# Kernel optimization log

Measured on AMD Instinct MI355X. Metric: run time of the kernel, lower is better.

Reference implementation:

```python
import jax, jax.numpy as jnp
import numpy as np

N = 100000
E = 1600000
D_IN = 128
D_H = 128
BN_EPS = 1e-5


def setup_inputs() -> dict:
    key = jax.random.key(0)
    ks = jax.random.split(key, 8)
    x = jax.random.normal(ks[0], (N, D_IN), dtype=jnp.float32)
    edge_index = jax.random.randint(ks[1], (2, E), 0, N, dtype=jnp.int64)
    # MLP params (Linear stores weight as [out, in])
    lim1 = 1.0 / np.sqrt(D_IN)
    W1 = jax.random.uniform(ks[2], (D_H, D_IN), minval=-lim1, maxval=lim1, dtype=jnp.float32)
    b1 = jax.random.uniform(ks[3], (D_H,), minval=-lim1, maxval=lim1, dtype=jnp.float32)
    gamma = jnp.ones((D_H,), dtype=jnp.float32)
    beta = jnp.zeros((D_H,), dtype=jnp.float32)
    lim2 = 1.0 / np.sqrt(D_H)
    W2 = jax.random.uniform(ks[4], (D_H, D_H), minval=-lim2, maxval=lim2, dtype=jnp.float32)
    b2 = jax.random.uniform(ks[5], (D_H,), minval=-lim2, maxval=lim2, dtype=jnp.float32)
    eps = jnp.float32(0.0)  # trainable eps parameter, init 0
    return {"x": x, "edge_index": edge_index, "eps": eps, "W1": W1, "b1": b1,
            "gamma": gamma, "beta": beta, "W2": W2, "b2": b2}


def reference(x, edge_index, eps, W1, b1, gamma, beta, W2, b2):
    src = edge_index[0]
    dst = edge_index[1]
    # Augmented edges = original + reversed + self-loops.
    # aggr[dst] += x[src]; aggr[src] += x[dst]; aggr[i] += x[i]
    aggr = jnp.zeros_like(x).at[dst].add(x[src]).at[src].add(x[dst]) + x
    h = (1.0 + eps) * x + aggr              # [N, D_IN]
    h = h @ W1.T + b1                        # [N, D_H]
    # BatchNorm1d in training mode: batch stats, biased variance
    mean = jnp.mean(h, axis=0)
    var = jnp.mean(jnp.square(h - mean), axis=0)
    h = gamma * (h - mean) * jax.lax.rsqrt(var + BN_EPS) + beta
    h = jax.nn.relu(h)
    return h @ W2.T + b2                     # [N, D_H]
```

## Files before the change

kernel.cpp:

```cpp
#include <hip/hip_runtime.h>
#include <hip/hip_fp16.h>

#define N_NODES 100000
#define EDGES   1600000
#define D       128
#define BN_EPS  1e-5f
#define TM      64
#define NT      ((N_NODES + TM - 1) / TM)
#define GGRID   782
#define NB      782
#define SLOT    4800
#define L1E     8
#define L1TILE  (256 * L1E)
#define GBLKS   1536
#define GWAVES  (GBLKS * 4)
#define NREP    32

typedef __attribute__((ext_vector_type(8))) short short8;
typedef __attribute__((ext_vector_type(4))) float f32x4;

__device__ __forceinline__ unsigned short bf_hi(float f) {
    unsigned u = __float_as_uint(f);
    unsigned t = u + 0x7FFF + ((u >> 16) & 1);
    return (unsigned short)(t >> 16);
}
__device__ __forceinline__ float bf_val(unsigned short h) {
    return __uint_as_float(((unsigned)h) << 16);
}
__device__ __forceinline__ void split8(const float* __restrict__ p, short8* hi, short8* lo) {
    short8 h, l;
#pragma unroll
    for (int i = 0; i < 8; ++i) {
        float f = p[i];
        unsigned short hh = bf_hi(f);
        ((unsigned short*)&h)[i] = (short)hh;
        ((unsigned short*)&l)[i] = (short)bf_hi(f - bf_val(hh));
    }
    *hi = h; *lo = l;
}

__launch_bounds__(256)
__global__ void fused_pg(const float* __restrict__ x,
                         const float* __restrict__ W1,
                         __half* __restrict__ yh,
                         const int* __restrict__ ei, int* __restrict__ gcur,
                         int* __restrict__ pairs) {
    __shared__ unsigned short sH[TM][136];
    __shared__ unsigned short sL[TM][136];
    const int tid = threadIdx.x;

    if (blockIdx.x >= GGRID) {
        int* cnt   = (int*)&sH[0][0];
        int* cbase = cnt + NB;
        for (int i = tid; i < NB; i += 256) cnt[i] = 0;
        __syncthreads();

        int bbA[L1E], rrA[L1E], pkA[L1E];
        int bbB[L1E], rrB[L1E], pkB[L1E];
        const int t0 = (blockIdx.x - GGRID) * L1TILE + tid;
#pragma unroll
        for (int j = 0; j < L1E; ++j) {
            int t = t0 + j * 256;
            bbA[j] = -1;
            bbB[j] = -1;
            if (t < EDGES) {
                int s = ei[t];
                int d = ei[EDGES + t];
                bbA[j] = d >> 7;
                pkA[j] = ((d & 127) << 17) | s;
                rrA[j] = atomicAdd(&cnt[bbA[j]], 1);
                bbB[j] = s >> 7;
                pkB[j] = ((s & 127) << 17) | d;
                rrB[j] = atomicAdd(&cnt[bbB[j]], 1);
            }
        }
        __syncthreads();
        for (int i = tid; i < NB; i += 256) {
            int c = cnt[i];
            cbase[i] = c ? (i * SLOT + atomicAdd(&gcur[i], c)) : 0;
        }
        __syncthreads();
#pragma unroll
        for (int j = 0; j < L1E; ++j) {
            if (bbA[j] >= 0) {
                pairs[cbase[bbA[j]] + rrA[j]] = pkA[j];
                pairs[cbase[bbB[j]] + rrB[j]] = pkB[j];
            }
        }
        return;
    }

    const int wv  = tid >> 6;
    const int ln  = tid & 63;
    const int lc  = ln & 15;
    const int qd  = ln >> 4;
    const int sr  = tid >> 5;
    const int sc4 = tid & 31;

    short8 Bh[4][2], Bl[4][2];
#pragma unroll
    for (int kk = 0; kk < 4; ++kk)
#pragma unroll
        for (int tl = 0; tl < 2; ++tl) {
            int woff = (wv * 32 + tl * 16 + lc) * D + kk * 32 + qd * 8;
            split8(W1 + woff, &Bh[kk][tl], &Bl[kk][tl]);
        }

    float4 pf[8];
    int tile = blockIdx.x;
#pragma unroll
    for (int i = 0; i < 8; ++i) {
        int gr = tile * TM + sr + i * 8;
        pf[i] = make_float4(0.f, 0.f, 0.f, 0.f);
        if (gr < N_NODES)
            pf[i] = *(const float4*)(x + (long long)gr * D + sc4 * 4);
    }

    while (tile < NT) {
#pragma unroll
        for (int i = 0; i < 8; ++i) {
            float4 v = pf[i];
            unsigned short h0 = bf_hi(v.x), h1b = bf_hi(v.y), h2 = bf_hi(v.z), h3 = bf_hi(v.w);
            unsigned short l0 = bf_hi(v.x - bf_val(h0)), l1 = bf_hi(v.y - bf_val(h1b));
            unsigned short l2 = bf_hi(v.z - bf_val(h2)), l3 = bf_hi(v.w - bf_val(h3));
            int r = sr + i * 8;
            *(uint2*)&sH[r][sc4 * 4] = make_uint2((unsigned)h0 | ((unsigned)h1b << 16),
                                                  (unsigned)h2 | ((unsigned)h3 << 16));
            *(uint2*)&sL[r][sc4 * 4] = make_uint2((unsigned)l0 | ((unsigned)l1 << 16),
                                                  (unsigned)l2 | ((unsigned)l3 << 16));
        }
        __syncthreads();
        int nxt = tile + GGRID;
        if (nxt < NT) {
#pragma unroll
            for (int i = 0; i < 8; ++i) {
                int gr = nxt * TM + sr + i * 8;
                pf[i] = make_float4(0.f, 0.f, 0.f, 0.f);
                if (gr < N_NODES)
                    pf[i] = *(const float4*)(x + (long long)gr * D + sc4 * 4);
            }
        }

        f32x4 acc[4][2];
#pragma unroll
        for (int m = 0; m < 4; ++m)
#pragma unroll
            for (int tl = 0; tl < 2; ++tl) acc[m][tl] = (f32x4){0.f, 0.f, 0.f, 0.f};

#pragma unroll
        for (int kk = 0; kk < 4; ++kk) {
#pragma unroll
            for (int m = 0; m < 4; ++m) {
                short8 ah = *(const short8*)&sH[m * 16 + lc][kk * 32 + qd * 8];
                short8 al = *(const short8*)&sL[m * 16 + lc][kk * 32 + qd * 8];
#pragma unroll
                for (int tl = 0; tl < 2; ++tl) {
                    acc[m][tl] = __builtin_amdgcn_mfma_f32_16x16x32_bf16(ah, Bh[kk][tl], acc[m][tl], 0, 0, 0);
                    acc[m][tl] = __builtin_amdgcn_mfma_f32_16x16x32_bf16(al, Bh[kk][tl], acc[m][tl], 0, 0, 0);
                    acc[m][tl] = __builtin_amdgcn_mfma_f32_16x16x32_bf16(ah, Bl[kk][tl], acc[m][tl], 0, 0, 0);
                }
            }
        }

        const int row0 = tile * TM;
#pragma unroll
        for (int m = 0; m < 4; ++m)
#pragma unroll
            for (int tl = 0; tl < 2; ++tl) {
                int col = wv * 32 + tl * 16 + lc;
#pragma unroll
                for (int r = 0; r < 4; ++r) {
                    int grow = row0 + m * 16 + qd * 4 + r;
                    if (grow < N_NODES)
                        yh[(long long)grow * D + col] = __float2half(acc[m][tl][r]);
                }
            }
        __syncthreads();
        tile = nxt;
    }
}

__launch_bounds__(256)
__global__ void bucket_fill(int* __restrict__ pairs, const int* __restrict__ gcur,
                            int* __restrict__ ofs, int* __restrict__ oen) {
    __shared__ int sP[SLOT];
    __shared__ int lc[128];
    __shared__ int cur[128];
    const int b    = blockIdx.x;
    const int tid  = threadIdx.x;
    const int base = b * SLOT;
    const int m    = min(gcur[b], SLOT);
    for (int i = tid; i < m; i += 256) sP[i] = pairs[base + i];
    if (tid < 128) lc[tid] = 0;
    __syncthreads();
    for (int i = tid; i < m; i += 256) atomicAdd(&lc[sP[i] >> 17], 1);
    __syncthreads();
    int v = (tid < 128) ? lc[tid] : 0;
    for (int d = 1; d < 128; d <<= 1) {
        int u = (tid >= d && tid < 128) ? lc[tid - d] : 0;
        __syncthreads();
        if (tid < 128) lc[tid] += u;
        __syncthreads();
    }
    if (tid < 128) {
        int abs0 = base + lc[tid] - v;
        cur[tid] = abs0;
        const int n = (b << 7) + tid;
        if (n < N_NODES) { ofs[n] = abs0; oen[n] = abs0 + v; }
    }
    __syncthreads();
    for (int i = tid; i < m; i += 256) {
        int p = sP[i];
        int r = atomicAdd(&cur[p >> 17], 1);
        pairs[r] = p & 0x1FFFF;
    }
}

__launch_bounds__(256)
__global__ void gather_aggr(const __half* __restrict__ yh,
                            const int* __restrict__ adj, const int* __restrict__ ofs,
                            const int* __restrict__ oen, const float* __restrict__ eps_p,
                            const float* __restrict__ b1,
                            float* __restrict__ h1, float* __restrict__ stats) {
    const int wv   = threadIdx.x >> 6;
    const int lane = threadIdx.x & 63;
    const int wave = blockIdx.x * 4 + wv;
    const __half2* xp = (const __half2*)yh;
    const float sc = 2.0f + eps_p[0];
    const float2 b1c = ((const float2*)b1)[lane];
    float sx = 0.f, sy = 0.f, qx = 0.f, qy = 0.f;

    for (int node = wave; node < N_NODES; node += GWAVES) {
        int b = ofs[node];
        int e = oen[node];
        float ax = 0.f, ay = 0.f;
        int i = b;
        for (; i + 8 <= e; i += 8) {
            int n0 = adj[i],     n1 = adj[i + 1], n2 = adj[i + 2], n3 = adj[i + 3];
            int n4 = adj[i + 4], n5 = adj[i + 5], n6 = adj[i + 6], n7 = adj[i + 7];
            __half2 v0 = xp[(unsigned)n0 * 64u + lane];
            __half2 v1 = xp[(unsigned)n1 * 64u + lane];
            __half2 v2 = xp[(unsigned)n2 * 64u + lane];
            __half2 v3 = xp[(unsigned)n3 * 64u + lane];
            __half2 v4 = xp[(unsigned)n4 * 64u + lane];
            __half2 v5 = xp[(unsigned)n5 * 64u + lane];
            __half2 v6 = xp[(unsigned)n6 * 64u + lane];
            __half2 v7 = xp[(unsigned)n7 * 64u + lane];
            float2 f0 = __half22float2(v0);
            float2 f1 = __half22float2(v1);
            float2 f2 = __half22float2(v2);
            float2 f3 = __half22float2(v3);
            float2 f4 = __half22float2(v4);
            float2 f5 = __half22float2(v5);
            float2 f6 = __half22float2(v6);
            float2 f7 = __half22float2(v7);
            ax += ((f0.x + f1.x) + (f2.x + f3.x)) + ((f4.x + f5.x) + (f6.x + f7.x));
            ay += ((f0.y + f1.y) + (f2.y + f3.y)) + ((f4.y + f5.y) + (f6.y + f7.y));
        }
        for (; i + 4 <= e; i += 4) {
            int n0 = adj[i], n1 = adj[i + 1], n2 = adj[i + 2], n3 = adj[i + 3];
            __half2 v0 = xp[(unsigned)n0 * 64u + lane];
            __half2 v1 = xp[(unsigned)n1 * 64u + lane];
            __half2 v2 = xp[(unsigned)n2 * 64u + lane];
            __half2 v3 = xp[(unsigned)n3 * 64u + lane];
            float2 f0 = __half22float2(v0);
            float2 f1 = __half22float2(v1);
            float2 f2 = __half22float2(v2);
            float2 f3 = __half22float2(v3);
            ax += (f0.x + f1.x) + (f2.x + f3.x);
            ay += (f0.y + f1.y) + (f2.y + f3.y);
        }
        for (; i < e; ++i) {
            __half2 v = xp[(unsigned)adj[i] * 64u + lane];
            float2 f = __half22float2(v);
            ax += f.x;
            ay += f.y;
        }
        float2 ys = __half22float2(xp[(unsigned)node * 64u + lane]);
        float ox = fmaf(sc, ys.x, ax) + b1c.x;
        float oy = fmaf(sc, ys.y, ay) + b1c.y;
        ((float2*)h1)[(long long)node * 64 + lane] = make_float2(ox, oy);
        sx += ox; sy += oy;
        qx += ox * ox; qy += oy * oy;
    }

    __shared__ float4 red[4][64];
    red[wv][lane] = make_float4(sx, sy, qx, qy);
    __syncthreads();
    if (wv == 0) {
        float4 a = red[0][lane], b4 = red[1][lane], c = red[2][lane], d4 = red[3][lane];
        float fx = (a.x + b4.x) + (c.x + d4.x);
        float fy = (a.y + b4.y) + (c.y + d4.y);
        float gx = (a.z + b4.z) + (c.z + d4.z);
        float gy = (a.w + b4.w) + (c.w + d4.w);
        float* st = stats + (blockIdx.x & (NREP - 1)) * 256;
        atomicAdd(&st[2 * lane],       fx);
        atomicAdd(&st[2 * lane + 1],   fy);
        atomicAdd(&st[128 + 2 * lane],     gx);
        atomicAdd(&st[128 + 2 * lane + 1], gy);
    }
}

__launch_bounds__(256)
__global__ void gemm2_mfma(float* __restrict__ h1out,
                           const float* __restrict__ W2,
                           const float* __restrict__ b2, const float* __restrict__ stats,
                           const float* __restrict__ gamma, const float* __restrict__ beta) {
    __shared__ unsigned short sH[TM][136];
    __shared__ unsigned short sL[TM][136];
    __shared__ float sScale[128];
    __shared__ float sShift[128];
    const int tid = threadIdx.x;
    const int wv  = tid >> 6;
    const int ln  = tid & 63;
    const int lc  = ln & 15;
    const int qd  = ln >> 4;
    const int sr  = tid >> 5;
    const int sc4 = tid & 31;

    if (tid < 128) {
        float s = 0.f, q = 0.f;
#pragma unroll
        for (int r = 0; r < NREP; ++r) {
            s += stats[r * 256 + tid];
            q += stats[r * 256 + 128 + tid];
        }
        float mean = s * (1.0f / N_NODES);
        float var  = fmaxf(q * (1.0f / N_NODES) - mean * mean, 0.0f);
        float sc   = gamma[tid] * rsqrtf(var + BN_EPS);
        sScale[tid] = sc;
        sShift[tid] = beta[tid] - mean * sc;
    }

    short8 Bh[4][2], Bl[4][2];
#pragma unroll
    for (int kk = 0; kk < 4; ++kk)
#pragma unroll
        for (int tl = 0; tl < 2; ++tl) {
            int woff = (wv * 32 + tl * 16 + lc) * D + kk * 32 + qd * 8;
            split8(W2 + woff, &Bh[kk][tl], &Bl[kk][tl]);
        }
    float bb[2];
    bb[0] = b2[wv * 32 + lc];
    bb[1] = b2[wv * 32 + 16 + lc];

    __syncthreads();

    float4 pf[8];
    int tile = blockIdx.x;
#pragma unroll
    for (int i = 0; i < 8; ++i) {
        int gr = tile * TM + sr + i * 8;
        pf[i] = make_float4(0.f, 0.f, 0.f, 0.f);
        if (gr < N_NODES)
            pf[i] = *(const float4*)(h1out + (long long)gr * D + sc4 * 4);
    }

    while (tile < NT) {
        float4 scv = *(const float4*)&sScale[sc4 * 4];
        float4 shv = *(const float4*)&sShift[sc4 * 4];
#pragma unroll
        for (int i = 0; i < 8; ++i) {
            int gr = tile * TM + sr + i * 8;
            float4 v = pf[i];
            if (gr < N_NODES) {
                v.x = fmaxf(0.f, fmaf(v.x, scv.x, shv.x));
                v.y = fmaxf(0.f, fmaf(v.y, scv.y, shv.y));
                v.z = fmaxf(0.f, fmaf(v.z, scv.z, shv.z));
                v.w = fmaxf(0.f, fmaf(v.w, scv.w, shv.w));
            } else {
                v = make_float4(0.f, 0.f, 0.f, 0.f);
            }
            unsigned short h0 = bf_hi(v.x), h1b = bf_hi(v.y), h2 = bf_hi(v.z), h3 = bf_hi(v.w);
            unsigned short l0 = bf_hi(v.x - bf_val(h0)), l1 = bf_hi(v.y - bf_val(h1b));
            unsigned short l2 = bf_hi(v.z - bf_val(h2)), l3 = bf_hi(v.w - bf_val(h3));
            int r = sr + i * 8;
            *(uint2*)&sH[r][sc4 * 4] = make_uint2((unsigned)h0 | ((unsigned)h1b << 16),
                                                  (unsigned)h2 | ((unsigned)h3 << 16));
            *(uint2*)&sL[r][sc4 * 4] = make_uint2((unsigned)l0 | ((unsigned)l1 << 16),
                                                  (unsigned)l2 | ((unsigned)l3 << 16));
        }
        __syncthreads();
        int nxt = tile + GGRID;
        if (nxt < NT) {
#pragma unroll
            for (int i = 0; i < 8; ++i) {
                int gr = nxt * TM + sr + i * 8;
                pf[i] = make_float4(0.f, 0.f, 0.f, 0.f);
                if (gr < N_NODES)
                    pf[i] = *(const float4*)(h1out + (long long)gr * D + sc4 * 4);
            }
        }

        f32x4 acc[4][2];
#pragma unroll
        for (int m = 0; m < 4; ++m)
#pragma unroll
            for (int tl = 0; tl < 2; ++tl) acc[m][tl] = (f32x4){0.f, 0.f, 0.f, 0.f};

#pragma unroll
        for (int kk = 0; kk < 4; ++kk) {
#pragma unroll
            for (int m = 0; m < 4; ++m) {
                short8 ah = *(const short8*)&sH[m * 16 + lc][kk * 32 + qd * 8];
                short8 al = *(const short8*)&sL[m * 16 + lc][kk * 32 + qd * 8];
#pragma unroll
                for (int tl = 0; tl < 2; ++tl) {
                    acc[m][tl] = __builtin_amdgcn_mfma_f32_16x16x32_bf16(ah, Bh[kk][tl], acc[m][tl], 0, 0, 0);
                    acc[m][tl] = __builtin_amdgcn_mfma_f32_16x16x32_bf16(al, Bh[kk][tl], acc[m][tl], 0, 0, 0);
                    acc[m][tl] = __builtin_amdgcn_mfma_f32_16x16x32_bf16(ah, Bl[kk][tl], acc[m][tl], 0, 0, 0);
                }
            }
        }

        const int row0 = tile * TM;
#pragma unroll
        for (int m = 0; m < 4; ++m)
#pragma unroll
            for (int tl = 0; tl < 2; ++tl) {
                int col = wv * 32 + tl * 16 + lc;
#pragma unroll
                for (int r = 0; r < 4; ++r) {
                    int grow = row0 + m * 16 + qd * 4 + r;
                    if (grow < N_NODES)
                        h1out[(long long)grow * D + col] = acc[m][tl][r] + bb[tl];
                }
            }
        __syncthreads();
        tile = nxt;
    }
}

extern "C" void kernel_launch(void* const* d_in, const int* in_sizes, int n_in,
                              void* d_out, int out_size, void* d_ws, size_t ws_size,
                              hipStream_t stream) {
    const float* x     = (const float*)d_in[0];
    const int*   ei    = (const int*)d_in[1];
    const float* eps_p = (const float*)d_in[2];
    const float* W1    = (const float*)d_in[3];
    const float* b1    = (const float*)d_in[4];
    const float* gamma = (const float*)d_in[5];
    const float* beta  = (const float*)d_in[6];
    const float* W2    = (const float*)d_in[7];
    const float* b2    = (const float*)d_in[8];

    __half* yh   = (__half*)d_ws;
    float*  stats = (float*)(yh + (long long)N_NODES * D);
    int*    gcur  = (int*)(stats + NREP * 256);
    int*    ofs   = gcur + 1024;
    int*    oen   = ofs + N_NODES;
    int*    pairs = (int*)(oen + N_NODES);
    int*    adj   = pairs;

    float* out = (float*)d_out;

    hipMemsetAsync(stats, 0, (NREP * 256 + 1024) * sizeof(int), stream);

    {
        fused_pg<<<GGRID + 782, 256, 0, stream>>>(x, W1, yh, ei, gcur, pairs);
    }
    {
        bucket_fill<<<NB, 256, 0, stream>>>(pairs, gcur, ofs, oen);
    }
    {
        gather_aggr<<<GBLKS, 256, 0, stream>>>(yh, adj, ofs, oen, eps_p, b1, out, stats);
    }
    {
        gemm2_mfma<<<GGRID, 256, 0, stream>>>(out, W2, b2, stats, gamma, beta);
    }
}
```

Baseline: 334.3 us.

## Fuse bucket sort and neighbor gather into one kernel using shared-memory adjacency

Merges the bucket_fill and gather_aggr kernels. Each 512-thread block now counting-sorts its bucket's pairs into LDS and immediately gathers neighbor features for its 128 nodes from there. This removes one launch, the global write and re-read of the adjacency and offset arrays, and the ofs/oen buffers. In exchange, gather parallelism is fixed at one block per 128 nodes (8 waves with 16 nodes each) rather than 1536 grid-strided blocks, which may lower memory-level parallelism and worsen load balance.

```diff
diff --git a/kernel.cpp b/kernel.cpp
--- a/kernel.cpp
+++ b/kernel.cpp
@@ -12,8 +12,6 @@
 #define SLOT    4800
 #define L1E     8
 #define L1TILE  (256 * L1E)
-#define GBLKS   1536
-#define GWAVES  (GBLKS * 4)
 #define NREP    32
 
 typedef __attribute__((ext_vector_type(8))) short short8;
@@ -180,20 +178,32 @@
     }
 }
 
-__launch_bounds__(256)
-__global__ void bucket_fill(int* __restrict__ pairs, const int* __restrict__ gcur,
-                            int* __restrict__ ofs, int* __restrict__ oen) {
-    __shared__ int sP[SLOT];
+__launch_bounds__(512)
+__global__ void bucket_gather(const __half* __restrict__ yh,
+                              const int* __restrict__ pairs, const int* __restrict__ gcur,
+                              const float* __restrict__ eps_p, const float* __restrict__ b1,
+                              float* __restrict__ h1, float* __restrict__ stats) {
+    __shared__ int sA[SLOT];
     __shared__ int lc[128];
     __shared__ int cur[128];
+    __shared__ int nofs[129];
+    __shared__ float4 red[8][64];
     const int b    = blockIdx.x;
     const int tid  = threadIdx.x;
     const int base = b * SLOT;
     const int m    = min(gcur[b], SLOT);
-    for (int i = tid; i < m; i += 256) sP[i] = pairs[base + i];
+
+    int my[10];
+#pragma unroll
+    for (int k = 0; k < 10; ++k) {
+        int i = tid + k * 512;
+        my[k] = (i < m) ? pairs[base + i] : -1;
+    }
     if (tid < 128) lc[tid] = 0;
     __syncthreads();
-    for (int i = tid; i < m; i += 256) atomicAdd(&lc[sP[i] >> 17], 1);
+#pragma unroll
+    for (int k = 0; k < 10; ++k)
+        if (my[k] >= 0) atomicAdd(&lc[my[k] >> 17], 1);
     __syncthreads();
     int v = (tid < 128) ? lc[tid] : 0;
     for (int d = 1; d < 128; d <<= 1) {
@@ -203,41 +213,37 @@
         __syncthreads();
     }
     if (tid < 128) {
-        int abs0 = base + lc[tid] - v;
-        cur[tid] = abs0;
-        const int n = (b << 7) + tid;
-        if (n < N_NODES) { ofs[n] = abs0; oen[n] = abs0 + v; }
-    }
-    __syncthreads();
-    for (int i = tid; i < m; i += 256) {
-        int p = sP[i];
-        int r = atomicAdd(&cur[p >> 17], 1);
-        pairs[r] = p & 0x1FFFF;
-    }
-}
-
-__launch_bounds__(256)
-__global__ void gather_aggr(const __half* __restrict__ yh,
-                            const int* __restrict__ adj, const int* __restrict__ ofs,
-                            const int* __restrict__ oen, const float* __restrict__ eps_p,
-                            const float* __restrict__ b1,
-                            float* __restrict__ h1, float* __restrict__ stats) {
-    const int wv   = threadIdx.x >> 6;
-    const int lane = threadIdx.x & 63;
-    const int wave = blockIdx.x * 4 + wv;
+        int e0 = lc[tid] - v;
+        cur[tid]  = e0;
+        nofs[tid] = e0;
+        if (tid == 127) nofs[128] = lc[127];
+    }
+    __syncthreads();
+#pragma unroll
+    for (int k = 0; k < 10; ++k)
+        if (my[k] >= 0) {
+            int r = atomicAdd(&cur[my[k] >> 17], 1);
+            sA[r] = my[k] & 0x1FFFF;
+        }
+    __syncthreads();
+
+    const int wv   = tid >> 6;
+    const int lane = tid & 63;
     const __half2* xp = (const __half2*)yh;
     const float sc = 2.0f + eps_p[0];
     const float2 b1c = ((const float2*)b1)[lane];
     float sx = 0.f, sy = 0.f, qx = 0.f, qy = 0.f;
 
-    for (int node = wave; node < N_NODES; node += GWAVES) {
-        int b = ofs[node];
-        int e = oen[node];
+    for (int ln = wv * 16; ln < wv * 16 + 16; ++ln) {
+        int node = (b << 7) + ln;
+        if (node >= N_NODES) break;
+        int nb = nofs[ln];
+        int ne = nofs[ln + 1];
         float ax = 0.f, ay = 0.f;
-        int i = b;
-        for (; i + 8 <= e; i += 8) {
-            int n0 = adj[i],     n1 = adj[i + 1], n2 = adj[i + 2], n3 = adj[i + 3];
-            int n4 = adj[i + 4], n5 = adj[i + 5], n6 = adj[i + 6], n7 = adj[i + 7];
+        int i = nb;
+        for (; i + 8 <= ne; i += 8) {
+            int n0 = sA[i],     n1 = sA[i + 1], n2 = sA[i + 2], n3 = sA[i + 3];
+            int n4 = sA[i + 4], n5 = sA[i + 5], n6 = sA[i + 6], n7 = sA[i + 7];
             __half2 v0 = xp[(unsigned)n0 * 64u + lane];
             __half2 v1 = xp[(unsigned)n1 * 64u + lane];
             __half2 v2 = xp[(unsigned)n2 * 64u + lane];
@@ -257,8 +263,8 @@
             ax += ((f0.x + f1.x) + (f2.x + f3.x)) + ((f4.x + f5.x) + (f6.x + f7.x));
             ay += ((f0.y + f1.y) + (f2.y + f3.y)) + ((f4.y + f5.y) + (f6.y + f7.y));
         }
-        for (; i + 4 <= e; i += 4) {
-            int n0 = adj[i], n1 = adj[i + 1], n2 = adj[i + 2], n3 = adj[i + 3];
+        for (; i + 4 <= ne; i += 4) {
+            int n0 = sA[i], n1 = sA[i + 1], n2 = sA[i + 2], n3 = sA[i + 3];
             __half2 v0 = xp[(unsigned)n0 * 64u + lane];
             __half2 v1 = xp[(unsigned)n1 * 64u + lane];
             __half2 v2 = xp[(unsigned)n2 * 64u + lane];
@@ -270,9 +276,9 @@
             ax += (f0.x + f1.x) + (f2.x + f3.x);
             ay += (f0.y + f1.y) + (f2.y + f3.y);
         }
-        for (; i < e; ++i) {
-            __half2 v = xp[(unsigned)adj[i] * 64u + lane];
-            float2 f = __half22float2(v);
+        for (; i < ne; ++i) {
+            __half2 vv = xp[(unsigned)sA[i] * 64u + lane];
+            float2 f = __half22float2(vv);
             ax += f.x;
             ay += f.y;
         }
@@ -284,18 +290,18 @@
         qx += ox * ox; qy += oy * oy;
     }
 
-    __shared__ float4 red[4][64];
     red[wv][lane] = make_float4(sx, sy, qx, qy);
     __syncthreads();
     if (wv == 0) {
-        float4 a = red[0][lane], b4 = red[1][lane], c = red[2][lane], d4 = red[3][lane];
-        float fx = (a.x + b4.x) + (c.x + d4.x);
-        float fy = (a.y + b4.y) + (c.y + d4.y);
-        float gx = (a.z + b4.z) + (c.z + d4.z);
-        float gy = (a.w + b4.w) + (c.w + d4.w);
-        float* st = stats + (blockIdx.x & (NREP - 1)) * 256;
-        atomicAdd(&st[2 * lane],       fx);
-        atomicAdd(&st[2 * lane + 1],   fy);
+        float fx = 0.f, fy = 0.f, gx = 0.f, gy = 0.f;
+#pragma unroll
+        for (int w = 0; w < 8; ++w) {
+            float4 a = red[w][lane];
+            fx += a.x; fy += a.y; gx += a.z; gy += a.w;
+        }
+        float* st = stats + (b & (NREP - 1)) * 256;
+        atomicAdd(&st[2 * lane],           fx);
+        atomicAdd(&st[2 * lane + 1],       fy);
         atomicAdd(&st[128 + 2 * lane],     gx);
         atomicAdd(&st[128 + 2 * lane + 1], gy);
     }
@@ -447,10 +453,7 @@
     __half* yh   = (__half*)d_ws;
     float*  stats = (float*)(yh + (long long)N_NODES * D);
     int*    gcur  = (int*)(stats + NREP * 256);
-    int*    ofs   = gcur + 1024;
-    int*    oen   = ofs + N_NODES;
-    int*    pairs = (int*)(oen + N_NODES);
-    int*    adj   = pairs;
+    int*    pairs = gcur + 1024;
 
     float* out = (float*)d_out;
 
@@ -460,10 +463,7 @@
         fused_pg<<<GGRID + 782, 256, 0, stream>>>(x, W1, yh, ei, gcur, pairs);
     }
     {
-        bucket_fill<<<NB, 256, 0, stream>>>(pairs, gcur, ofs, oen);
-    }
-    {
-        gather_aggr<<<GBLKS, 256, 0, stream>>>(yh, adj, ofs, oen, eps_p, b1, out, stats);
+        bucket_gather<<<NB, 512, 0, stream>>>(yh, pairs, gcur, eps_p, b1, out, stats);
     }
     {
         gemm2_mfma<<<GGRID, 256, 0, stream>>>(out, W2, b2, stats, gamma, beta);
```

New measurement: 324.0 us. 3.1% less time.
